# Optimization experiments

Hardware: AMD Instinct MI355X
Metric: run time of the kernel (lower is better)

The kernel has to match this reference:

```python
import jax, jax.numpy as jnp
import numpy as np

TAU = [1, 2, 4, 8]
B, T, FC, FX = 128, 2048, 512, 512


def setup_inputs() -> dict:
    key = jax.random.key(0)
    k1, k2, k3, k4 = jax.random.split(key, 4)
    C = jax.random.normal(k1, (B, T, FC), dtype=jnp.float32)
    X = jax.random.normal(k2, (B, T, FX), dtype=jnp.float32)
    # one Linear(encoding_size -> context_size) per tau; torch weight layout [out, in]
    W = jax.random.normal(k3, (len(TAU), FC, FX), dtype=jnp.float32) * (1.0 / np.sqrt(FX))
    b = jax.random.normal(k4, (len(TAU), FC), dtype=jnp.float32) * 0.01
    return {"C": C, "X": X, "W": W, "b": b}


def _infonce(Ct, Xe, Wk, bk):
    # Ct: [B, Tt, fc], Xe: [B, Tt, fx]
    Xt = jnp.einsum('btf,gf->btg', Xe, Wk) + bk          # Linear: [B, Tt, fc]
    Z = jnp.einsum('itf,jtf->ijt', Ct, Xt)               # scores [B, B, Tt]
    Zmax = jnp.max(Z, axis=1, keepdims=True)             # [B, 1, Tt]
    lse = jnp.log(jnp.sum(jnp.exp(Z - Zmax), axis=1)) + Zmax[:, 0]  # [B, Tt]
    Zdiag = jnp.diagonal(Z, axis1=0, axis2=1).T          # Z[i,i,t] -> [B, Tt]
    return jnp.mean(Zdiag - lse)


def reference(C, X, W, b):
    losses = [_infonce(C[:, :-t], X[:, t:], W[k], b[k]) for k, t in enumerate(TAU)]
    return jnp.stack(losses)
```

## Files before the change

kernel.cpp:

```cpp
#include <hip/hip_runtime.h>
#include <math.h>

constexpr int Tn  = 2048;
constexpr int FCn = 512;
constexpr int FXn = 512;
constexpr int SXW = 72;
constexpr int SYC = 136;
constexpr int SZS = 132;

typedef __attribute__((ext_vector_type(8))) short  bf16x8;
typedef __attribute__((ext_vector_type(4))) float  f32x4;

__device__ __forceinline__ unsigned pk2(float a, float b) {
  return __builtin_amdgcn_perm(__float_as_uint(b), __float_as_uint(a), 0x07060302u);
}
__device__ __forceinline__ uint4 pack8(float4 a, float4 b) {
  uint4 rv;
  rv.x = pk2(a.x, a.y); rv.y = pk2(a.z, a.w);
  rv.z = pk2(b.x, b.y); rv.w = pk2(b.z, b.w);
  return rv;
}

__global__ void zero4(float* out) {
  if (threadIdx.x < 4) out[threadIdx.x] = 0.0f;
}

__global__ void finalize4(float* out) {
  int k = threadIdx.x;
  if (k < 4) out[k] *= 1.0f / (128.0f * (float)(Tn - (1 << k)));
}

__global__ void tobf16(const float* __restrict__ s, unsigned short* __restrict__ d) {
  int i = blockIdx.x * 256 + threadIdx.x;
  float4 v = ((const float4*)s)[i];
  uint2 p; p.x = pk2(v.x, v.y); p.y = pk2(v.z, v.w);
  ((uint2*)d)[i] = p;
}

template <bool CBF>
__global__ __launch_bounds__(512, 4)
void infonce_bf16(const void* __restrict__ Cany, const unsigned short* __restrict__ Xb,
                  const unsigned short* __restrict__ Wb, float* __restrict__ out)
{
  __shared__ __align__(16) unsigned char smem[71680];
  unsigned short* sX = (unsigned short*)(smem);
  unsigned short* sW = (unsigned short*)(smem + 18432);
  unsigned short* sY = (unsigned short*)(smem + 36864);
  float* sZ   = (float*)(smem);
  float* sRed = (float*)(smem + 67584);

  const int tid  = threadIdx.x;
  const int lane = tid & 63;
  const int wave = tid >> 6;
  const int r    = lane & 15;
  const int h    = lane >> 4;
  const int wr   = wave >> 1;
  const int wc   = wave & 1;

  const int orig = blockIdx.x;
  const int xcd  = orig & 7;
  const int loc  = orig >> 3;
  const int wg   = (xcd < 4) ? (xcd * 1024 + loc) : (4096 + (xcd - 4) * 1023 + loc);
  const int k    = wg & 3;
  const int t    = wg >> 2;
  const int tau  = 1 << k;
  if (t >= Tn - tau) return;

  const int srow = tid >> 2;
  const int scol = (tid & 3) * 16;
  const unsigned short* xs = Xb + (size_t)srow * (Tn * FXn)
                             + (size_t)(t + tau) * FXn + scol;
  const unsigned short* ws = Wb + (size_t)k * (FCn * FXn) + (size_t)srow * FXn + scol;
  unsigned short* xd = sX + srow * SXW + scol;
  unsigned short* wd = sW + srow * SXW + scol;

  const unsigned short* c0h = nullptr; const unsigned short* c1h = nullptr;
  const float*          c0f = nullptr; const float*          c1f = nullptr;
  if constexpr (CBF) {
    c0h = (const unsigned short*)Cany + (size_t)(wr * 32 + r) * (Tn * FCn)
          + (size_t)t * FCn;
    c1h = c0h + (size_t)16 * (Tn * FCn);
  } else {
    c0f = (const float*)Cany + (size_t)(wr * 32 + r) * (Tn * FCn) + (size_t)t * FCn;
    c1f = c0f + (size_t)16 * (Tn * FCn);
  }

  uint4 px0, px1, pw0, pw1;

#define LOAD_X(XC) do { \
    const uint4* _p = (const uint4*)(xs + (XC) * 64); \
    px0 = _p[0]; px1 = _p[1]; } while (0)
#define LOAD_W(GC, XC) do { \
    const uint4* _p = (const uint4*)(ws + (size_t)((GC) * 128) * FXn + (XC) * 64); \
    pw0 = _p[0]; pw1 = _p[1]; } while (0)
#define STORE_XW() do { \
    *(uint4*)(xd) = px0; *(uint4*)(xd + 8) = px1; \
    *(uint4*)(wd) = pw0; *(uint4*)(wd + 8) = pw1; } while (0)
#define MFMA_Y() do { \
    _Pragma("unroll") \
    for (int ks = 0; ks < 2; ++ks) { \
      const int xoo = ks * 32 + h * 8; \
      bf16x8 a0 = *(const bf16x8*)(sX + (wr * 32 + 0  + r) * SXW + xoo); \
      bf16x8 a1 = *(const bf16x8*)(sX + (wr * 32 + 16 + r) * SXW + xoo); \
      _Pragma("unroll") \
      for (int bg = 0; bg < 4; ++bg) { \
        bf16x8 bb = *(const bf16x8*)(sW + (wc * 64 + bg * 16 + r) * SXW + xoo); \
        yacc[0][bg] = __builtin_amdgcn_mfma_f32_16x16x32_bf16(a0, bb, yacc[0][bg], 0, 0, 0); \
        yacc[1][bg] = __builtin_amdgcn_mfma_f32_16x16x32_bf16(a1, bb, yacc[1][bg], 0, 0, 0); \
      } } } while (0)

  f32x4 zacc[2][4];
#pragma unroll
  for (int a = 0; a < 2; ++a)
#pragma unroll
    for (int b = 0; b < 4; ++b) zacc[a][b] = f32x4{0.f, 0.f, 0.f, 0.f};

  LOAD_X(0); LOAD_W(0, 0);

  for (int gc = 0; gc < 4; ++gc) {
    f32x4 yacc[2][4];
#pragma unroll
    for (int a = 0; a < 2; ++a)
#pragma unroll
      for (int b = 0; b < 4; ++b) yacc[a][b] = f32x4{0.f, 0.f, 0.f, 0.f};

#pragma unroll 1
    for (int xc = 0; xc < 8; ++xc) {
      __syncthreads();
      STORE_XW();
      __syncthreads();
      if (xc < 7)      { LOAD_X(xc + 1); LOAD_W(gc, xc + 1); }
      else if (gc < 3) { LOAD_X(0);      LOAD_W(gc + 1, 0); }
      MFMA_Y();
    }

#pragma unroll
    for (int aj = 0; aj < 2; ++aj)
#pragma unroll
      for (int bg = 0; bg < 4; ++bg)
#pragma unroll
        for (int reg = 0; reg < 4; ++reg)
          sY[(wr * 32 + aj * 16 + h * 4 + reg) * SYC + (wc * 64 + bg * 16 + r)] =
              (unsigned short)(__float_as_uint(yacc[aj][bg][reg]) >> 16);
    __syncthreads();

#pragma unroll
    for (int ks = 0; ks < 4; ++ks) {
      const int go = ks * 32 + h * 8;
      bf16x8 a0, a1;
      if constexpr (CBF) {
        a0 = *(const bf16x8*)(c0h + gc * 128 + go);
        a1 = *(const bf16x8*)(c1h + gc * 128 + go);
      } else {
        float4 ca = *(const float4*)(c0f + gc * 128 + go);
        float4 cb = *(const float4*)(c0f + gc * 128 + go + 4);
        float4 cc = *(const float4*)(c1f + gc * 128 + go);
        float4 cd = *(const float4*)(c1f + gc * 128 + go + 4);
        a0 = __builtin_bit_cast(bf16x8, pack8(ca, cb));
        a1 = __builtin_bit_cast(bf16x8, pack8(cc, cd));
      }
#pragma unroll
      for (int bj = 0; bj < 4; ++bj) {
        bf16x8 bb = *(const bf16x8*)(sY + (wc * 64 + bj * 16 + r) * SYC + go);
        zacc[0][bj] = __builtin_amdgcn_mfma_f32_16x16x32_bf16(a0, bb, zacc[0][bj], 0, 0, 0);
        zacc[1][bj] = __builtin_amdgcn_mfma_f32_16x16x32_bf16(a1, bb, zacc[1][bj], 0, 0, 0);
      }
    }
  }
  __syncthreads();
#pragma unroll
  for (int ai = 0; ai < 2; ++ai)
#pragma unroll
    for (int bj = 0; bj < 4; ++bj)
#pragma unroll
      for (int reg = 0; reg < 4; ++reg)
        sZ[(wr * 32 + ai * 16 + h * 4 + reg) * SZS + (wc * 64 + bj * 16 + r)] =
            zacc[ai][bj][reg];
  __syncthreads();

  const int row = wave * 16 + (lane >> 2);
  const int c0l = lane & 3;
  float mx = -3.4e38f;
#pragma unroll
  for (int m = 0; m < 32; ++m) mx = fmaxf(mx, sZ[row * SZS + c0l + m * 4]);
  mx = fmaxf(mx, __shfl_xor(mx, 1));
  mx = fmaxf(mx, __shfl_xor(mx, 2));
  float sum = 0.f;
#pragma unroll
  for (int m = 0; m < 32; ++m) sum += __expf(sZ[row * SZS + c0l + m * 4] - mx);
  sum += __shfl_xor(sum, 1);
  sum += __shfl_xor(sum, 2);
  float val = (c0l == 0) ? (sZ[row * SZS + row] - (__logf(sum) + mx)) : 0.f;
#pragma unroll
  for (int off = 1; off < 64; off <<= 1) val += __shfl_xor(val, off);
  if (lane == 0) sRed[wave] = val;
  __syncthreads();
  if (tid == 0) {
    float bs = 0.f;
#pragma unroll
    for (int w2 = 0; w2 < 8; ++w2) bs += sRed[w2];
    atomicAdd(out + k, bs);
  }
#undef LOAD_X
#undef LOAD_W
#undef STORE_XW
#undef MFMA_Y
}

template <bool WBF>
__global__ __launch_bounds__(512, 4)
void infonce_main(const float* __restrict__ Cp, const float* __restrict__ Xp,
                  const void* __restrict__ Wp, float* __restrict__ out)
{
  __shared__ __align__(16) unsigned char smem[71680];
  unsigned short* sX = (unsigned short*)(smem);
  unsigned short* sW = (unsigned short*)(smem + 18432);
  unsigned short* sY = (unsigned short*)(smem + 36864);
  unsigned short* sC = (unsigned short*)(smem);
  float* sZ   = (float*)(smem);
  float* sRed = (float*)(smem + 67584);

  const int tid  = threadIdx.x;
  const int lane = tid & 63;
  const int wave = tid >> 6;
  const int r    = lane & 15;
  const int h    = lane >> 4;
  const int wr   = wave >> 1;
  const int wc   = wave & 1;

  const int orig = blockIdx.x;
  const int xcd  = orig & 7;
  const int loc  = orig >> 3;
  const int wg   = (xcd < 4) ? (xcd * 1024 + loc) : (4096 + (xcd - 4) * 1023 + loc);
  const int k    = wg & 3;
  const int t    = wg >> 2;
  const int tau  = 1 << k;
  if (t >= Tn - tau) return;

  const float* Cb = Cp + (size_t)t * FCn;
  const float* Xb = Xp + (size_t)(t + tau) * FXn;

  const int srow = tid >> 2;
  const int scol = (tid & 3) * 16;
  const float* xs = Xb + (size_t)srow * (Tn * FXn) + scol;
  unsigned short* xd = sX + srow * SXW + scol;
  unsigned short* wd = sW + srow * SXW + scol;
  const unsigned short* wsh = (const unsigned short*)Wp + (size_t)k * (FCn * FXn)
                              + (size_t)srow * FXn + scol;
  const float* wsf = (const float*)Wp + (size_t)k * (FCn * FXn)
                     + (size_t)srow * FXn + scol;
  const int crow0 = tid >> 4;
  const int ccol  = (tid & 15) * 8;
  const float* cs = Cb + (size_t)crow0 * (Tn * FCn) + ccol;
  unsigned short* cd = sC + crow0 * SYC + ccol;
  const size_t cstep = (size_t)32 * Tn * FCn;

  float4 px0, px1, px2, px3;
  float4 pw0, pw1, pw2, pw3;
  uint4  pb0, pb1;
  float4 pc0, pc1, pc2, pc3, pc4, pc5, pc6, pc7;

#define LOAD_X(XC) do { \
    const float4* _p = (const float4*)(xs + (XC) * 64); \
    px0 = _p[0]; px1 = _p[1]; px2 = _p[2]; px3 = _p[3]; } while (0)
#define LOAD_W(GC, XC) do { \
    if constexpr (WBF) { \
      const uint4* _p = (const uint4*)(wsh + (size_t)((GC) * 128) * FXn + (XC) * 64); \
      pb0 = _p[0]; pb1 = _p[1]; \
    } else { \
      const float4* _p = (const float4*)(wsf + (size_t)((GC) * 128) * FXn + (XC) * 64); \
      pw0 = _p[0]; pw1 = _p[1]; pw2 = _p[2]; pw3 = _p[3]; } } while (0)
#define STORE_XW() do { \
    *(uint4*)(xd)     = pack8(px0, px1); \
    *(uint4*)(xd + 8) = pack8(px2, px3); \
    if constexpr (WBF) { *(uint4*)(wd) = pb0; *(uint4*)(wd + 8) = pb1; } \
    else { *(uint4*)(wd) = pack8(pw0, pw1); *(uint4*)(wd + 8) = pack8(pw2, pw3); } \
  } while (0)
#define MFMA_Y() do { \
    _Pragma("unroll") \
    for (int ks = 0; ks < 2; ++ks) { \
      const int xoo = ks * 32 + h * 8; \
      bf16x8 a0 = *(const bf16x8*)(sX + (wr * 32 + 0  + r) * SXW + xoo); \
      bf16x8 a1 = *(const bf16x8*)(sX + (wr * 32 + 16 + r) * SXW + xoo); \
      _Pragma("unroll") \
      for (int bg = 0; bg < 4; ++bg) { \
        bf16x8 bb = *(const bf16x8*)(sW + (wc * 64 + bg * 16 + r) * SXW + xoo); \
        yacc[0][bg] = __builtin_amdgcn_mfma_f32_16x16x32_bf16(a0, bb, yacc[0][bg], 0, 0, 0); \
        yacc[1][bg] = __builtin_amdgcn_mfma_f32_16x16x32_bf16(a1, bb, yacc[1][bg], 0, 0, 0); \
      } } } while (0)

  f32x4 zacc[2][4];
#pragma unroll
  for (int a = 0; a < 2; ++a)
#pragma unroll
    for (int b = 0; b < 4; ++b) zacc[a][b] = f32x4{0.f, 0.f, 0.f, 0.f};

  LOAD_X(0); LOAD_W(0, 0);

  for (int gc = 0; gc < 4; ++gc) {
    f32x4 yacc[2][4];
#pragma unroll
    for (int a = 0; a < 2; ++a)
#pragma unroll
      for (int b = 0; b < 4; ++b) yacc[a][b] = f32x4{0.f, 0.f, 0.f, 0.f};

    for (int xc = 0; xc < 7; ++xc) {
      __syncthreads();
      STORE_XW();
      __syncthreads();
      LOAD_X(xc + 1); LOAD_W(gc, xc + 1);
      MFMA_Y();
    }
    __syncthreads();
    STORE_XW();
    __syncthreads();
    {
      const float4* p0 = (const float4*)(cs + 0 * cstep + gc * 128);
      const float4* p1 = (const float4*)(cs + 1 * cstep + gc * 128);
      const float4* p2 = (const float4*)(cs + 2 * cstep + gc * 128);
      const float4* p3 = (const float4*)(cs + 3 * cstep + gc * 128);
      pc0 = p0[0]; pc1 = p0[1];
      pc2 = p1[0]; pc3 = p1[1];
      pc4 = p2[0]; pc5 = p2[1];
      pc6 = p3[0]; pc7 = p3[1];
    }
    MFMA_Y();

#pragma unroll
    for (int aj = 0; aj < 2; ++aj)
#pragma unroll
      for (int bg = 0; bg < 4; ++bg)
#pragma unroll
        for (int reg = 0; reg < 4; ++reg)
          sY[(wr * 32 + aj * 16 + h * 4 + reg) * SYC + (wc * 64 + bg * 16 + r)] =
              (unsigned short)(__float_as_uint(yacc[aj][bg][reg]) >> 16);
    __syncthreads();
    *(uint4*)(cd + 0 * 32 * SYC) = pack8(pc0, pc1);
    *(uint4*)(cd + 1 * 32 * SYC) = pack8(pc2, pc3);
    *(uint4*)(cd + 2 * 32 * SYC) = pack8(pc4, pc5);
    *(uint4*)(cd + 3 * 32 * SYC) = pack8(pc6, pc7);
    __syncthreads();
    if (gc < 3) { LOAD_X(0); LOAD_W(gc + 1, 0); }
#pragma unroll
    for (int ks = 0; ks < 4; ++ks) {
      const int go = ks * 32 + h * 8;
      bf16x8 a0 = *(const bf16x8*)(sC + (wr * 32 + 0  + r) * SYC + go);
      bf16x8 a1 = *(const bf16x8*)(sC + (wr * 32 + 16 + r) * SYC + go);
#pragma unroll
      for (int bj = 0; bj < 4; ++bj) {
        bf16x8 bb = *(const bf16x8*)(sY + (wc * 64 + bj * 16 + r) * SYC + go);
        zacc[0][bj] = __builtin_amdgcn_mfma_f32_16x16x32_bf16(a0, bb, zacc[0][bj], 0, 0, 0);
        zacc[1][bj] = __builtin_amdgcn_mfma_f32_16x16x32_bf16(a1, bb, zacc[1][bj], 0, 0, 0);
      }
    }
  }
  __syncthreads();
#pragma unroll
  for (int ai = 0; ai < 2; ++ai)
#pragma unroll
    for (int bj = 0; bj < 4; ++bj)
#pragma unroll
      for (int reg = 0; reg < 4; ++reg)
        sZ[(wr * 32 + ai * 16 + h * 4 + reg) * SZS + (wc * 64 + bj * 16 + r)] =
            zacc[ai][bj][reg];
  __syncthreads();

  const int row = wave * 16 + (lane >> 2);
  const int c0l = lane & 3;
  float mx = -3.4e38f;
#pragma unroll
  for (int m = 0; m < 32; ++m) mx = fmaxf(mx, sZ[row * SZS + c0l + m * 4]);
  mx = fmaxf(mx, __shfl_xor(mx, 1));
  mx = fmaxf(mx, __shfl_xor(mx, 2));
  float sum = 0.f;
#pragma unroll
  for (int m = 0; m < 32; ++m) sum += __expf(sZ[row * SZS + c0l + m * 4] - mx);
  sum += __shfl_xor(sum, 1);
  sum += __shfl_xor(sum, 2);
  float val = (c0l == 0) ? (sZ[row * SZS + row] - (__logf(sum) + mx)) : 0.f;
#pragma unroll
  for (int off = 1; off < 64; off <<= 1) val += __shfl_xor(val, off);
  if (lane == 0) sRed[wave] = val;
  __syncthreads();
  if (tid == 0) {
    float bs = 0.f;
#pragma unroll
    for (int w2 = 0; w2 < 8; ++w2) bs += sRed[w2];
    atomicAdd(out + k, bs);
  }
#undef LOAD_X
#undef LOAD_W
#undef STORE_XW
#undef MFMA_Y
}

extern "C" void kernel_launch(void* const* d_in, const int* in_sizes, int n_in,
                              void* d_out, int out_size, void* d_ws, size_t ws_size,
                              hipStream_t stream) {
  const float* C = (const float*)d_in[0];
  const float* X = (const float*)d_in[1];
  const float* W = (const float*)d_in[2];
  float* out = (float*)d_out;

  const size_t NX = (size_t)128 * Tn * FXn;
  const size_t NW = (size_t)4 * FCn * FXn;
  const size_t WS_W    = NW * 2;
  const size_t WS_MID  = WS_W + NX * 2;
  const size_t WS_FULL = WS_MID + NX * 2;

  hipLaunchKernelGGL(zero4, dim3(1), dim3(64), 0, stream, out);

  if (ws_size >= WS_MID) {
    unsigned short* Wbf = (unsigned short*)d_ws;
    unsigned short* Xbf = (unsigned short*)((char*)d_ws + WS_W);
    hipLaunchKernelGGL(tobf16, dim3((unsigned)(NW / 1024)), dim3(256), 0, stream, W, Wbf);
    hipLaunchKernelGGL(tobf16, dim3((unsigned)(NX / 1024)), dim3(256), 0, stream, X, Xbf);
    if (ws_size >= WS_FULL) {
      unsigned short* Cbf = (unsigned short*)((char*)d_ws + WS_MID);
      hipLaunchKernelGGL(tobf16, dim3((unsigned)(NX / 1024)), dim3(256), 0, stream, C, Cbf);
      hipLaunchKernelGGL(infonce_bf16<true>, dim3(2047 * 4), dim3(512), 0, stream,
                         (const void*)Cbf, Xbf, Wbf, out);
    } else {
      hipLaunchKernelGGL(infonce_bf16<false>, dim3(2047 * 4), dim3(512), 0, stream,
                         (const void*)C, Xbf, Wbf, out);
    }
  } else if (ws_size >= WS_W) {
    hipLaunchKernelGGL(tobf16, dim3((unsigned)(NW / 1024)), dim3(256), 0, stream,
                       W, (unsigned short*)d_ws);
    hipLaunchKernelGGL(infonce_main<true>, dim3(2047 * 4), dim3(512), 0, stream,
                       C, X, (const void*)d_ws, out);
  } else {
    hipLaunchKernelGGL(infonce_main<false>, dim3(2047 * 4), dim3(512), 0, stream,
                       C, X, (const void*)W, out);
  }
  hipLaunchKernelGGL(finalize4, dim3(1), dim3(64), 0, stream, out);
}
```

Before: 1.455 ms.

## Shrink LDS footprint to double occupancy and read fp32 C directly

The main kernel's shared memory drops from about 70KB to about 37KB. The Y tile now aliases the X/W staging buffers, and the softmax reduction runs in two half-tile passes that reuse the same space. Launch bounds rise to allow eight workgroups per CU, and the separate C-to-bf16 conversion pass is removed, so fp32 C is converted in registers. This trades an extra barrier per gc step and an extra pass in the epilogue for more resident waves and one less full-tensor conversion kernel, with added register pressure as a risk.

Measured after the change: 4.261 ms. 193% more time.

```diff
diff --git a/kernel.cpp b/kernel.cpp
--- a/kernel.cpp
+++ b/kernel.cpp
@@ -37,17 +37,16 @@
   ((uint2*)d)[i] = p;
 }
 
-template <bool CBF>
-__global__ __launch_bounds__(512, 4)
-void infonce_bf16(const void* __restrict__ Cany, const unsigned short* __restrict__ Xb,
-                  const unsigned short* __restrict__ Wb, float* __restrict__ out)
+__global__ __launch_bounds__(512, 8)
+void infonce_v14(const float* __restrict__ Cp, const unsigned short* __restrict__ Xb,
+                 const unsigned short* __restrict__ Wb, float* __restrict__ out)
 {
-  __shared__ __align__(16) unsigned char smem[71680];
+  __shared__ __align__(16) unsigned char smem[36928];
   unsigned short* sX = (unsigned short*)(smem);
   unsigned short* sW = (unsigned short*)(smem + 18432);
-  unsigned short* sY = (unsigned short*)(smem + 36864);
-  float* sZ   = (float*)(smem);
-  float* sRed = (float*)(smem + 67584);
+  unsigned short* sY = (unsigned short*)(smem);
+  float* sZh  = (float*)(smem);
+  float* sRed = (float*)(smem + 36864);
 
   const int tid  = threadIdx.x;
   const int lane = tid & 63;
@@ -65,25 +64,19 @@
   const int t    = wg >> 2;
   const int tau  = 1 << k;
   if (t >= Tn - tau) return;
+  const int s = t + tau;
 
   const int srow = tid >> 2;
   const int scol = (tid & 3) * 16;
-  const unsigned short* xs = Xb + (size_t)srow * (Tn * FXn)
-                             + (size_t)(t + tau) * FXn + scol;
-  const unsigned short* ws = Wb + (size_t)k * (FCn * FXn) + (size_t)srow * FXn + scol;
+  const size_t xstr = (size_t)Tn * FXn;
+  const unsigned short* xs = Xb + (size_t)srow * xstr + (size_t)s * FXn + scol;
+  const unsigned short* wsh = Wb + (size_t)k * (FCn * FXn) + (size_t)srow * FXn + scol;
   unsigned short* xd = sX + srow * SXW + scol;
   unsigned short* wd = sW + srow * SXW + scol;
 
-  const unsigned short* c0h = nullptr; const unsigned short* c1h = nullptr;
-  const float*          c0f = nullptr; const float*          c1f = nullptr;
-  if constexpr (CBF) {
-    c0h = (const unsigned short*)Cany + (size_t)(wr * 32 + r) * (Tn * FCn)
-          + (size_t)t * FCn;
-    c1h = c0h + (size_t)16 * (Tn * FCn);
-  } else {
-    c0f = (const float*)Cany + (size_t)(wr * 32 + r) * (Tn * FCn) + (size_t)t * FCn;
-    c1f = c0f + (size_t)16 * (Tn * FCn);
-  }
+  const size_t cstr = (size_t)Tn * FCn;
+  const float* c0f = Cp + (size_t)(wr * 32 + r) * cstr + (size_t)t * FCn;
+  const float* c1f = c0f + (size_t)16 * cstr;
 
   uint4 px0, px1, pw0, pw1;
 
@@ -91,7 +84,7 @@
     const uint4* _p = (const uint4*)(xs + (XC) * 64); \
     px0 = _p[0]; px1 = _p[1]; } while (0)
 #define LOAD_W(GC, XC) do { \
-    const uint4* _p = (const uint4*)(ws + (size_t)((GC) * 128) * FXn + (XC) * 64); \
+    const uint4* _p = (const uint4*)(wsh + (size_t)((GC) * 128) * FXn + (XC) * 64); \
     pw0 = _p[0]; pw1 = _p[1]; } while (0)
 #define STORE_XW() do { \
     *(uint4*)(xd) = px0; *(uint4*)(xd + 8) = px1; \
@@ -117,6 +110,7 @@
 
   LOAD_X(0); LOAD_W(0, 0);
 
+#pragma unroll 1
   for (int gc = 0; gc < 4; ++gc) {
     f32x4 yacc[2][4];
 #pragma unroll
@@ -133,6 +127,7 @@
       else if (gc < 3) { LOAD_X(0);      LOAD_W(gc + 1, 0); }
       MFMA_Y();
     }
+    __syncthreads();
 
 #pragma unroll
     for (int aj = 0; aj < 2; ++aj)
@@ -147,18 +142,12 @@
 #pragma unroll
     for (int ks = 0; ks < 4; ++ks) {
       const int go = ks * 32 + h * 8;
-      bf16x8 a0, a1;
-      if constexpr (CBF) {
-        a0 = *(const bf16x8*)(c0h + gc * 128 + go);
-        a1 = *(const bf16x8*)(c1h + gc * 128 + go);
-      } else {
-        float4 ca = *(const float4*)(c0f + gc * 128 + go);
-        float4 cb = *(const float4*)(c0f + gc * 128 + go + 4);
-        float4 cc = *(const float4*)(c1f + gc * 128 + go);
-        float4 cd = *(const float4*)(c1f + gc * 128 + go + 4);
-        a0 = __builtin_bit_cast(bf16x8, pack8(ca, cb));
-        a1 = __builtin_bit_cast(bf16x8, pack8(cc, cd));
-      }
+      float4 ca = *(const float4*)(c0f + gc * 128 + go);
+      float4 cb = *(const float4*)(c0f + gc * 128 + go + 4);
+      float4 cc = *(const float4*)(c1f + gc * 128 + go);
+      float4 cd = *(const float4*)(c1f + gc * 128 + go + 4);
+      bf16x8 a0 = __builtin_bit_cast(bf16x8, pack8(ca, cb));
+      bf16x8 a1 = __builtin_bit_cast(bf16x8, pack8(cc, cd));
 #pragma unroll
       for (int bj = 0; bj < 4; ++bj) {
         bf16x8 bb = *(const bf16x8*)(sY + (wc * 64 + bj * 16 + r) * SYC + go);
@@ -168,29 +157,40 @@
     }
   }
   __syncthreads();
-#pragma unroll
-  for (int ai = 0; ai < 2; ++ai)
-#pragma unroll
-    for (int bj = 0; bj < 4; ++bj)
-#pragma unroll
-      for (int reg = 0; reg < 4; ++reg)
-        sZ[(wr * 32 + ai * 16 + h * 4 + reg) * SZS + (wc * 64 + bj * 16 + r)] =
-            zacc[ai][bj][reg];
-  __syncthreads();
-
-  const int row = wave * 16 + (lane >> 2);
-  const int c0l = lane & 3;
-  float mx = -3.4e38f;
-#pragma unroll
-  for (int m = 0; m < 32; ++m) mx = fmaxf(mx, sZ[row * SZS + c0l + m * 4]);
-  mx = fmaxf(mx, __shfl_xor(mx, 1));
-  mx = fmaxf(mx, __shfl_xor(mx, 2));
-  float sum = 0.f;
-#pragma unroll
-  for (int m = 0; m < 32; ++m) sum += __expf(sZ[row * SZS + c0l + m * 4] - mx);
-  sum += __shfl_xor(sum, 1);
-  sum += __shfl_xor(sum, 2);
-  float val = (c0l == 0) ? (sZ[row * SZS + row] - (__logf(sum) + mx)) : 0.f;
+
+  float val = 0.f;
+  const int rloc = wave * 8 + (lane >> 3);
+  const int c8   = lane & 7;
+#pragma unroll 1
+  for (int p = 0; p < 2; ++p) {
+    if ((wave >> 2) == p) {
+      const int rl0 = (wr & 1) * 32;
+#pragma unroll
+      for (int ai = 0; ai < 2; ++ai)
+#pragma unroll
+        for (int bj = 0; bj < 4; ++bj)
+#pragma unroll
+          for (int reg = 0; reg < 4; ++reg)
+            sZh[(rl0 + ai * 16 + h * 4 + reg) * SZS + (wc * 64 + bj * 16 + r)] =
+                zacc[ai][bj][reg];
+    }
+    __syncthreads();
+    float mx = -3.4e38f;
+#pragma unroll
+    for (int m = 0; m < 16; ++m) mx = fmaxf(mx, sZh[rloc * SZS + c8 + m * 8]);
+    mx = fmaxf(mx, __shfl_xor(mx, 1));
+    mx = fmaxf(mx, __shfl_xor(mx, 2));
+    mx = fmaxf(mx, __shfl_xor(mx, 4));
+    float sum = 0.f;
+#pragma unroll
+    for (int m = 0; m < 16; ++m) sum += __expf(sZh[rloc * SZS + c8 + m * 8] - mx);
+    sum += __shfl_xor(sum, 1);
+    sum += __shfl_xor(sum, 2);
+    sum += __shfl_xor(sum, 4);
+    if (c8 == 0)
+      val += sZh[rloc * SZS + (p * 64 + rloc)] - (__logf(sum) + mx);
+    __syncthreads();
+  }
 #pragma unroll
   for (int off = 1; off < 64; off <<= 1) val += __shfl_xor(val, off);
   if (lane == 0) sRed[wave] = val;
@@ -276,7 +276,7 @@
     if constexpr (WBF) { *(uint4*)(wd) = pb0; *(uint4*)(wd + 8) = pb1; } \
     else { *(uint4*)(wd) = pack8(pw0, pw1); *(uint4*)(wd + 8) = pack8(pw2, pw3); } \
   } while (0)
-#define MFMA_Y() do { \
+#define MFMA_YF() do { \
     _Pragma("unroll") \
     for (int ks = 0; ks < 2; ++ks) { \
       const int xoo = ks * 32 + h * 8; \
@@ -309,7 +309,7 @@
       STORE_XW();
       __syncthreads();
       LOAD_X(xc + 1); LOAD_W(gc, xc + 1);
-      MFMA_Y();
+      MFMA_YF();
     }
     __syncthreads();
     STORE_XW();
@@ -324,7 +324,7 @@
       pc4 = p2[0]; pc5 = p2[1];
       pc6 = p3[0]; pc7 = p3[1];
     }
-    MFMA_Y();
+    MFMA_YF();
 
 #pragma unroll
     for (int aj = 0; aj < 2; ++aj)
@@ -391,7 +391,7 @@
 #undef LOAD_X
 #undef LOAD_W
 #undef STORE_XW
-#undef MFMA_Y
+#undef MFMA_YF
 }
 
 extern "C" void kernel_launch(void* const* d_in, const int* in_sizes, int n_in,
@@ -404,9 +404,8 @@
 
   const size_t NX = (size_t)128 * Tn * FXn;
   const size_t NW = (size_t)4 * FCn * FXn;
-  const size_t WS_W    = NW * 2;
-  const size_t WS_MID  = WS_W + NX * 2;
-  const size_t WS_FULL = WS_MID + NX * 2;
+  const size_t WS_W   = NW * 2;
+  const size_t WS_MID = WS_W + NX * 2;
 
   hipLaunchKernelGGL(zero4, dim3(1), dim3(64), 0, stream, out);
 
@@ -415,15 +414,8 @@
     unsigned short* Xbf = (unsigned short*)((char*)d_ws + WS_W);
     hipLaunchKernelGGL(tobf16, dim3((unsigned)(NW / 1024)), dim3(256), 0, stream, W, Wbf);
     hipLaunchKernelGGL(tobf16, dim3((unsigned)(NX / 1024)), dim3(256), 0, stream, X, Xbf);
-    if (ws_size >= WS_FULL) {
-      unsigned short* Cbf = (unsigned short*)((char*)d_ws + WS_MID);
-      hipLaunchKernelGGL(tobf16, dim3((unsigned)(NX / 1024)), dim3(256), 0, stream, C, Cbf);
-      hipLaunchKernelGGL(infonce_bf16<true>, dim3(2047 * 4), dim3(512), 0, stream,
-                         (const void*)Cbf, Xbf, Wbf, out);
-    } else {
-      hipLaunchKernelGGL(infonce_bf16<false>, dim3(2047 * 4), dim3(512), 0, stream,
-                         (const void*)C, Xbf, Wbf, out);
-    }
+    hipLaunchKernelGGL(infonce_v14, dim3(2047 * 4), dim3(512), 0, stream,
+                       C, Xbf, Wbf, out);
   } else if (ws_size >= WS_W) {
     hipLaunchKernelGGL(tobf16, dim3((unsigned)(NW / 1024)), dim3(256), 0, stream,
                        W, (unsigned short*)d_ws);
```
